# Performance work log

Hardware: AMD Instinct MI355X
Metric: run time of the kernel (lower is better)

## Reference

```python
import jax, jax.numpy as jnp
import numpy as np

HEADS = 16
DIM_HEAD = 64
SCALE = DIM_HEAD ** -0.5


def setup_inputs() -> dict:
    key = jax.random.key(0)
    ks = jax.random.split(key, 6)
    d = 1024
    x = jax.random.normal(ks[0], (4, 2048, d), dtype=jnp.float32)
    s = d ** -0.5
    Wq = jax.random.normal(ks[1], (d, d), dtype=jnp.float32) * s
    Wk = jax.random.normal(ks[2], (d, d), dtype=jnp.float32) * s
    Wv = jax.random.normal(ks[3], (d, d), dtype=jnp.float32) * s
    Wo = jax.random.normal(ks[4], (d, d), dtype=jnp.float32) * s
    bo = jnp.zeros((d,), dtype=jnp.float32)
    return {"x": x, "Wq": Wq, "Wk": Wk, "Wv": Wv, "Wo": Wo, "bo": bo}


def reference(x, Wq, Wk, Wv, Wo, bo):
    b, n, _ = x.shape
    h, dh = HEADS, DIM_HEAD
    # projections (bias-free), split heads: b n (h d) -> b h n d
    def split(t):
        return t.reshape(b, n, h, dh).transpose(0, 2, 1, 3)
    q = split(x @ Wq.T)
    k = split(x @ Wk.T)
    v = split(x @ Wv.T)
    # fp32 scores (inputs already fp32; explicit cast mirrors ATTN_PRECISION='fp32')
    sim = jnp.einsum('bhid,bhjd->bhij', q.astype(jnp.float32), k.astype(jnp.float32)) * SCALE
    attn = jax.nn.softmax(sim, axis=-1)
    out = jnp.einsum('bhij,bhjd->bhid', attn, v)
    out = out.transpose(0, 2, 1, 3).reshape(b, n, h * dh)
    return out @ Wo.T + bo
```

## Files before the change

kernel.cpp:

```cpp
#include <hip/hip_runtime.h>

typedef float f32x4 __attribute__((ext_vector_type(4)));
typedef float f32x16 __attribute__((ext_vector_type(16)));
typedef short s16x8 __attribute__((ext_vector_type(8)));
typedef __bf16 bf16x8 __attribute__((ext_vector_type(8)));
typedef unsigned int u32;
typedef unsigned int u32x4 __attribute__((ext_vector_type(4)));
typedef unsigned short u16;

struct __align__(8) us4 { u16 s[4]; };

#define DEVINL static __device__ __forceinline__

DEVINL f32x4 mfma_bf16(s16x8 a, s16x8 b, f32x4 c) {
  return __builtin_amdgcn_mfma_f32_16x16x32_bf16(
      __builtin_bit_cast(bf16x8, a), __builtin_bit_cast(bf16x8, b), c, 0, 0, 0);
}

DEVINL f32x16 mfma32_bf16(s16x8 a, s16x8 b, f32x16 c) {
  return __builtin_amdgcn_mfma_f32_32x32x16_bf16(
      __builtin_bit_cast(bf16x8, a), __builtin_bit_cast(bf16x8, b), c, 0, 0, 0);
}

DEVINL u16 f2bf(float f) {
  __bf16 h = (__bf16)f;
  return __builtin_bit_cast(u16, h);
}

DEVINL u32 pk2(float a, float b) {
  return (u32)f2bf(a) | ((u32)f2bf(b) << 16);
}

DEVINL void pl32swap(u32& a, u32& b) {
  asm volatile("v_permlane32_swap_b32 %0, %1" : "+v"(a), "+v"(b));
}

DEVINL float exp2_fast(float x) {
  float r;
  asm("v_exp_f32 %0, %1" : "=v"(r) : "v"(x));
  return r;
}

#define GLD16(gp, lp)                                                         \
  __builtin_amdgcn_global_load_lds(                                           \
      (const __attribute__((address_space(1))) void*)(gp),                    \
      (__attribute__((address_space(3))) void*)(lp), 16, 0, 0)

#define SCHEDB() __builtin_amdgcn_sched_barrier(0)

#define WAITV(n)                                                              \
  do {                                                                        \
    asm volatile("s_waitcnt vmcnt(" #n ")" ::: "memory");                     \
    SCHEDB();                                                                 \
  } while (0)

#define BARRIER()                                                             \
  do {                                                                        \
    SCHEDB();                                                                 \
    __builtin_amdgcn_s_barrier();                                             \
    SCHEDB();                                                                 \
  } while (0)

__global__ __launch_bounds__(256) void convert_k(
    const float* __restrict__ x, const float* __restrict__ wq,
    const float* __restrict__ wk, const float* __restrict__ wv,
    const float* __restrict__ wo, u16* __restrict__ xb,
    u16* __restrict__ wqkv, u16* __restrict__ wob) {
  long i = (long)blockIdx.x * 256 + threadIdx.x;
  const float4* s;
  u16* d;
  if (i < 2097152) {
    s = (const float4*)x + i; d = xb + i * 4;
  } else if (i < 2359296) {
    long j = i - 2097152; s = (const float4*)wq + j; d = wqkv + j * 4;
  } else if (i < 2621440) {
    long j = i - 2359296; s = (const float4*)wk + j; d = wqkv + 1048576 + j * 4;
  } else if (i < 2883584) {
    long j = i - 2621440; s = (const float4*)wv + j; d = wqkv + 2097152 + j * 4;
  } else {
    long j = i - 2883584; s = (const float4*)wo + j; d = wob + j * 4;
  }
  float4 v = *s;
  us4 w;
  w.s[0] = f2bf(v.x); w.s[1] = f2bf(v.y); w.s[2] = f2bf(v.z); w.s[3] = f2bf(v.w);
  *(us4*)d = w;
}

template <int MODE>
__global__ __launch_bounds__(256, 4) void gemm_bt(
    const u16* __restrict__ A, const u16* __restrict__ B,
    u16* __restrict__ oq, u16* __restrict__ ok, u16* __restrict__ ovt,
    float* __restrict__ oc, const float* __restrict__ bias) {
  __shared__ __align__(16) u16 lA[128 * 64];
  __shared__ __align__(16) u16 lB[128 * 64];
  const int t = threadIdx.x;
  const int wave = t >> 6, lane = t & 63, g = lane >> 4, c = lane & 15;
  const int NBN = (MODE == 0) ? 24 : 8;
  const int wg = blockIdx.x;
  const int cpx = gridDim.x >> 3;
  const int wgp = (wg & 7) * cpx + (wg >> 3);
  const int bm = wgp / NBN, bn = wgp % NBN;
  const int wr = wave >> 1, wc = wave & 1;
  f32x4 acc[4][4] = {};
  const long arow0 = (long)bm * 128;
  const long brow0 = (long)bn * 128;

  for (int kk = 0; kk < 1024; kk += 64) {
    __syncthreads();
#pragma unroll
    for (int i = 0; i < 4; ++i) {
      int s = i * 256 + t;
      int row = s >> 3, ch = s & 7;
      int gc = (ch ^ (row & 7)) * 8;
      GLD16(A + (arow0 + row) * 1024 + kk + gc, lA + (i * 256 + wave * 64) * 8);
      GLD16(B + (brow0 + row) * 1024 + kk + gc, lB + (i * 256 + wave * 64) * 8);
    }
    __syncthreads();
#pragma unroll
    for (int k2 = 0; k2 < 2; ++k2) {
      s16x8 af[4], bfr[4];
#pragma unroll
      for (int m = 0; m < 4; ++m) {
        int r = wr * 64 + m * 16 + c;
        af[m] = *(const s16x8*)&lA[r * 64 + (((k2 * 4 + g) ^ (r & 7)) * 8)];
      }
#pragma unroll
      for (int n = 0; n < 4; ++n) {
        int r = wc * 64 + n * 16 + c;
        bfr[n] = *(const s16x8*)&lB[r * 64 + (((k2 * 4 + g) ^ (r & 7)) * 8)];
      }
#pragma unroll
      for (int m = 0; m < 4; ++m)
#pragma unroll
        for (int n = 0; n < 4; ++n)
          acc[m][n] = mfma_bf16(af[m], bfr[n], acc[m][n]);
    }
  }

  if (MODE == 0) {
    const float SQ = 0.18033688011112042f;
#pragma unroll
    for (int n = 0; n < 4; ++n) {
      int colb = bn * 128 + wc * 64 + n * 16;
      int tsel = colb >> 10;
      int f = colb & 1023;
      int h = f >> 6, d0 = f & 63;
#pragma unroll
      for (int m = 0; m < 4; ++m) {
        int row = bm * 128 + wr * 64 + m * 16 + g * 4;
        int b = row >> 11, nn = row & 2047;
        if (tsel == 0) {
          long base = ((long)(b * 16 + h) * 2048 + nn) * 64 + d0 + c;
#pragma unroll
          for (int j = 0; j < 4; ++j)
            oq[base + (long)j * 64] = f2bf(acc[m][n][j] * SQ);
        } else if (tsel == 1) {
          long base = ((long)(b * 16 + h) * 2048 + nn) * 64 + d0 + c;
#pragma unroll
          for (int j = 0; j < 4; ++j)
            ok[base + (long)j * 64] = f2bf(acc[m][n][j]);
        } else {
          us4 w;
#pragma unroll
          for (int j = 0; j < 4; ++j) w.s[j] = f2bf(acc[m][n][j]);
          *(us4*)&ovt[((long)(b * 16 + h) * 64 + d0 + c) * 2048 + nn] = w;
        }
      }
    }
  } else {
#pragma unroll
    for (int n = 0; n < 4; ++n) {
      int col = bn * 128 + wc * 64 + n * 16 + c;
      float bv = bias[col];
#pragma unroll
      for (int m = 0; m < 4; ++m) {
        int row = bm * 128 + wr * 64 + m * 16 + g * 4;
#pragma unroll
        for (int j = 0; j < 4; ++j)
          oc[(long)(row + j) * 1024 + col] = acc[m][n][j] + bv;
      }
    }
  }
}

__global__ __launch_bounds__(256, 4) void flash_attn(
    const u16* __restrict__ q, const u16* __restrict__ k,
    const u16* __restrict__ vt, u16* __restrict__ ao) {
  __shared__ __align__(16) u16 lds[20480];
  u16* const Kb[3] = {lds, lds + 4096, lds + 8192};
  u16* const Vb[2] = {lds + 12288, lds + 16384};
  const int t = threadIdx.x;
  const int wave = t >> 6, lane = t & 63;
  const int lc = lane & 31, hi = lane >> 5, x7 = lc & 7;
  const int wg = blockIdx.x;
  const int bh = wg & 63, qt = wg >> 6;

  const u16* kb = k + (long)bh * (2048 * 64);
  const u16* vb = vt + (long)bh * (64 * 2048);

  const int srow = t >> 3, sch = t & 7;
  const int sgc = (sch ^ (srow & 7)) * 8;
  const u16* kp = kb + srow * 64 + sgc;
  const u16* vp = vb + srow * 2048 + sgc;

  auto stageK = [&](u16* kd) {
    GLD16(kp, kd + wave * 512);
    GLD16(kp + 2048, kd + 2048 + wave * 512);
    kp += 4096;
  };
  auto stageV = [&](u16* vd) {
    GLD16(vp, vd + wave * 512);
    GLD16(vp + 65536, vd + 2048 + wave * 512);
    vp += 64;
  };

  const u16* qp =
      q + ((long)bh * 2048 + qt * 128 + wave * 32 + lc) * 64 + hi * 8;
  s16x8 bq[4];
#pragma unroll
  for (int kd = 0; kd < 4; ++kd) bq[kd] = *(const s16x8*)(qp + kd * 16);

  float ls = 0.f;
  f32x16 o[2] = {};

  auto qkt = [&](const u16* kB, f32x16 (&st)[2]) {
    __builtin_amdgcn_s_setprio(1);
#pragma unroll
    for (int ks = 0; ks < 2; ++ks)
#pragma unroll
      for (int kd = 0; kd < 4; ++kd) {
        s16x8 ak =
            *(const s16x8*)&kB[(ks * 32 + lc) * 64 + (((kd * 2 + hi) ^ x7) * 8)];
        st[ks] = mfma32_bf16(ak, bq[kd], st[ks]);
      }
    __builtin_amdgcn_s_setprio(0);
  };

  auto softmax = [&](f32x16 (&st)[2]) {
    float ps = 0.f;
#pragma unroll
    for (int ks = 0; ks < 2; ++ks)
#pragma unroll
      for (int i = 0; i < 16; ++i) {
        float p = exp2_fast(st[ks][i]);
        st[ks][i] = p;
        ps += p;
      }
    ps += __shfl_xor(ps, 32);
    ls += ps;
  };

  auto pv = [&](const u16* vB, f32x16 (&st)[2]) {
    __builtin_amdgcn_s_setprio(1);
#pragma unroll
    for (int ks2 = 0; ks2 < 4; ++ks2) {
      const f32x16& P = st[ks2 >> 1];
      const int b0 = (ks2 & 1) * 8;
      u32 A0 = pk2(P[b0 + 0], P[b0 + 1]);
      u32 B0 = pk2(P[b0 + 2], P[b0 + 3]);
      u32 A1 = pk2(P[b0 + 4], P[b0 + 5]);
      u32 B1 = pk2(P[b0 + 6], P[b0 + 7]);
      pl32swap(A0, A1);
      pl32swap(B0, B1);
      u32x4 pw;
      pw[0] = A0; pw[1] = B0; pw[2] = A1; pw[3] = B1;
      s16x8 bp = __builtin_bit_cast(s16x8, pw);
#pragma unroll
      for (int do2 = 0; do2 < 2; ++do2) {
        s16x8 av = *(const s16x8*)&vB[(do2 * 32 + lc) * 64 +
                                      (((ks2 * 2 + hi) ^ x7) * 8)];
        o[do2] = mfma32_bf16(av, bp, o[do2]);
      }
    }
    __builtin_amdgcn_s_setprio(0);
  };

  stageV(Vb[0]);
  stageK(Kb[0]);
  stageK(Kb[1]);
  WAITV(2);
  BARRIER();

  u16 *kcur = Kb[0], *knext = Kb[1], *kthird = Kb[2];
  u16 *vcur = Vb[0], *vother = Vb[1];

#pragma unroll 6
  for (int t2 = 0; t2 < 30; ++t2) {
    stageV(vother);
    stageK(kthird);
    f32x16 st[2] = {};
    qkt(kcur, st);
    softmax(st);
    pv(vcur, st);
    WAITV(2);
    BARRIER();
    u16* tmp = kcur;
    kcur = knext; knext = kthird; kthird = tmp;
    tmp = vcur; vcur = vother; vother = tmp;
  }
  {
    stageV(vother);
    f32x16 st[2] = {};
    qkt(kcur, st);
    softmax(st);
    pv(vcur, st);
    WAITV(0);
    BARRIER();
  }
  {
    f32x16 st[2] = {};
    qkt(knext, st);
    softmax(st);
    pv(vother, st);
  }

  int b = bh >> 4, h = bh & 15;
  u16* ob = ao + ((long)b * 2048 + qt * 128 + wave * 32 + lc) * 1024 + h * 64 +
            hi * 4;
  float inv = 1.0f / ls;
#pragma unroll
  for (int do2 = 0; do2 < 2; ++do2)
#pragma unroll
    for (int tq = 0; tq < 4; ++tq) {
      us4 w;
#pragma unroll
      for (int j = 0; j < 4; ++j) w.s[j] = f2bf(o[do2][tq * 4 + j] * inv);
      *(us4*)&ob[do2 * 32 + tq * 8] = w;
    }
}

extern "C" void kernel_launch(void* const* d_in, const int* in_sizes, int n_in,
                              void* d_out, int out_size, void* d_ws, size_t ws_size,
                              hipStream_t stream) {
  const float* x = (const float*)d_in[0];
  const float* wq = (const float*)d_in[1];
  const float* wk = (const float*)d_in[2];
  const float* wv = (const float*)d_in[3];
  const float* wo = (const float*)d_in[4];
  const float* bo = (const float*)d_in[5];
  char* ws = (char*)d_ws;
  u16* xb   = (u16*)(ws);
  u16* wqkv = (u16*)(ws + (16l << 20));
  u16* wob  = (u16*)(ws + (22l << 20));
  u16* qb   = (u16*)(ws + (24l << 20));
  u16* kbuf = (u16*)(ws + (40l << 20));
  u16* vtb  = (u16*)(ws + (56l << 20));
  u16* aob  = (u16*)(ws + (72l << 20));
  float* out = (float*)d_out;

  convert_k<<<12288, 256, 0, stream>>>(x, wq, wk, wv, wo, xb, wqkv, wob);
  gemm_bt<0><<<1536, 256, 0, stream>>>(xb, wqkv, qb, kbuf, vtb,
                                       nullptr, nullptr);
  flash_attn<<<1024, 256, 0, stream>>>(qb, kbuf, vtb, aob);
  gemm_bt<1><<<512, 256, 0, stream>>>(aob, wob, nullptr, nullptr,
                                      nullptr, out, bo);
}
```

Before: 175.1 us.

## Replace QKV projection GEMM with 256x256-tile double-buffered 8-wave kernel

Adds a new QKV projection kernel that uses 256x256 output tiles with 512 threads. It double-buffers LDS and interleaves direct global-to-LDS loads of the next K-tile with MFMA quadrants, using setprio around the MFMA blocks. The larger tiles are meant to raise arithmetic intensity and cut global/LDS traffic relative to the 128x128 kernel, with prefetch hiding load latency. In exchange the grid drops to 384 workgroups, each with 128 KB of LDS and many accumulator registers, which lowers occupancy and may leave the CUs unevenly loaded.

New measurement: 191.5 us. +9.4%, slower.

```diff
diff --git a/kernel.cpp b/kernel.cpp
--- a/kernel.cpp
+++ b/kernel.cpp
@@ -51,6 +51,12 @@
 #define WAITV(n)                                                              \
   do {                                                                        \
     asm volatile("s_waitcnt vmcnt(" #n ")" ::: "memory");                     \
+    SCHEDB();                                                                 \
+  } while (0)
+
+#define WAITL()                                                               \
+  do {                                                                        \
+    asm volatile("s_waitcnt lgkmcnt(0)" ::: "memory");                        \
     SCHEDB();                                                                 \
   } while (0)
 
@@ -86,6 +92,140 @@
   *(us4*)d = w;
 }
 
+__global__ __launch_bounds__(512, 2) void gemm256(
+    const u16* __restrict__ A, const u16* __restrict__ B,
+    u16* __restrict__ oq, u16* __restrict__ ok, u16* __restrict__ ovt) {
+  __shared__ __align__(16) u16 lA[2][256 * 64];
+  __shared__ __align__(16) u16 lB[2][256 * 64];
+  const int t = threadIdx.x;
+  const int wave = t >> 6, lane = t & 63, g = lane >> 4, c = lane & 15;
+  const int wm = wave >> 2, wn = wave & 3;
+  const int wg = blockIdx.x;
+  const int wgp = (wg & 7) * 48 + (wg >> 3);
+  const int bm = wgp / 12, bn = wgp % 12;
+
+  f32x4 acc[8][4] = {};
+
+  const int srow = t >> 3, sch = t & 7;
+  const int sgc = (sch ^ (srow & 7)) * 8;
+  const u16* abase = A + ((long)bm * 256 + srow) * 1024 + sgc;
+  const u16* bbase = B + ((long)bn * 256 + srow) * 1024 + sgc;
+  const int dbase = wave * 512;
+
+  const int x7 = c & 7;
+  const int kch0 = (g ^ x7) * 8;
+  const int kch1 = ((4 + g) ^ x7) * 8;
+
+  s16x8 aF[8][2], bF[4][2];
+
+  auto stageA = [&](int bi, int kk) {
+#pragma unroll
+    for (int h = 0; h < 2; ++h)
+#pragma unroll
+      for (int i = 0; i < 2; ++i)
+        GLD16(abase + (h * 128 + i * 64) * 1024 + kk,
+              &lA[bi][h * 8192 + i * 4096 + dbase]);
+  };
+  auto stageB = [&](int bi, int kk) {
+#pragma unroll
+    for (int h = 0; h < 2; ++h)
+#pragma unroll
+      for (int i = 0; i < 2; ++i)
+        GLD16(bbase + (h * 128 + i * 64) * 1024 + kk,
+              &lB[bi][h * 8192 + i * 4096 + dbase]);
+  };
+  auto readA = [&](int bi, int mh) {
+#pragma unroll
+    for (int m = 0; m < 4; ++m) {
+      int r = (wm * 128 + (mh * 4 + m) * 16 + c) * 64;
+      aF[mh * 4 + m][0] = *(const s16x8*)&lA[bi][r + kch0];
+      aF[mh * 4 + m][1] = *(const s16x8*)&lA[bi][r + kch1];
+    }
+  };
+  auto readB = [&](int bi, int nh) {
+#pragma unroll
+    for (int n = 0; n < 2; ++n) {
+      int r = (wn * 64 + (nh * 2 + n) * 16 + c) * 64;
+      bF[nh * 2 + n][0] = *(const s16x8*)&lB[bi][r + kch0];
+      bF[nh * 2 + n][1] = *(const s16x8*)&lB[bi][r + kch1];
+    }
+  };
+  auto quad = [&](int mh, int nh) {
+    __builtin_amdgcn_s_setprio(1);
+#pragma unroll
+    for (int m = 0; m < 4; ++m)
+#pragma unroll
+      for (int n = 0; n < 2; ++n)
+#pragma unroll
+        for (int ks = 0; ks < 2; ++ks)
+          acc[mh * 4 + m][nh * 2 + n] = mfma_bf16(
+              aF[mh * 4 + m][ks], bF[nh * 2 + n][ks], acc[mh * 4 + m][nh * 2 + n]);
+    __builtin_amdgcn_s_setprio(0);
+  };
+
+  stageA(0, 0);
+  stageB(0, 0);
+  WAITV(0);
+  BARRIER();
+
+#pragma unroll 1
+  for (int tile = 0; tile < 16; ++tile) {
+    const int bi = tile & 1;
+    const int kk = (tile + 1) * 64;
+    readA(bi, 0);
+    readB(bi, 0);
+    if (tile < 15) stageA(bi ^ 1, kk);
+    BARRIER();
+    WAITL();
+    quad(0, 0);
+    BARRIER();
+    readB(bi, 1);
+    if (tile < 15) stageB(bi ^ 1, kk);
+    BARRIER();
+    WAITL();
+    quad(0, 1);
+    BARRIER();
+    readA(bi, 1);
+    BARRIER();
+    WAITL();
+    quad(1, 0);
+    BARRIER();
+    quad(1, 1);
+    WAITV(0);
+    BARRIER();
+  }
+
+  const float SQ = 0.18033688011112042f;
+#pragma unroll
+  for (int N = 0; N < 4; ++N) {
+    int colb = bn * 256 + wn * 64 + N * 16;
+    int tsel = colb >> 10;
+    int f = colb & 1023;
+    int h = f >> 6, d0 = f & 63;
+#pragma unroll
+    for (int M = 0; M < 8; ++M) {
+      int row = bm * 256 + wm * 128 + M * 16 + g * 4;
+      int b = row >> 11, nn = row & 2047;
+      if (tsel == 0) {
+        long base = ((long)(b * 16 + h) * 2048 + nn) * 64 + d0 + c;
+#pragma unroll
+        for (int j = 0; j < 4; ++j)
+          oq[base + (long)j * 64] = f2bf(acc[M][N][j] * SQ);
+      } else if (tsel == 1) {
+        long base = ((long)(b * 16 + h) * 2048 + nn) * 64 + d0 + c;
+#pragma unroll
+        for (int j = 0; j < 4; ++j)
+          ok[base + (long)j * 64] = f2bf(acc[M][N][j]);
+      } else {
+        us4 w;
+#pragma unroll
+        for (int j = 0; j < 4; ++j) w.s[j] = f2bf(acc[M][N][j]);
+        *(us4*)&ovt[((long)(b * 16 + h) * 64 + d0 + c) * 2048 + nn] = w;
+      }
+    }
+  }
+}
+
 template <int MODE>
 __global__ __launch_bounds__(256, 4) void gemm_bt(
     const u16* __restrict__ A, const u16* __restrict__ B,
@@ -349,8 +489,7 @@
   float* out = (float*)d_out;
 
   convert_k<<<12288, 256, 0, stream>>>(x, wq, wk, wv, wo, xb, wqkv, wob);
-  gemm_bt<0><<<1536, 256, 0, stream>>>(xb, wqkv, qb, kbuf, vtb,
-                                       nullptr, nullptr);
+  gemm256<<<384, 512, 0, stream>>>(xb, wqkv, qb, kbuf, vtb);
   flash_attn<<<1024, 256, 0, stream>>>(qb, kbuf, vtb, aob);
   gemm_bt<1><<<512, 256, 0, stream>>>(aob, wob, nullptr, nullptr,
                                       nullptr, out, bo);
```
